# Optimization experiments

Hardware: AMD Instinct MI355X
Metric: run time of the kernel (lower is better)

## Reference

```python
import jax, jax.numpy as jnp
import numpy as np

B, C, H, W = 8, 512, 64, 64


def _conv1x1(x, w, b):
    # x: (B,C,H,W), w: (O,C,1,1) torch layout, b: (O,)
    y = jnp.einsum('bchw,oc->bohw', x, w[:, :, 0, 0])
    return y + b[None, :, None, None]


def setup_inputs() -> dict:
    key = jax.random.key(0)
    ks = jax.random.split(key, 9)
    s = 1.0 / np.sqrt(C)
    inp = {
        'x': jax.random.normal(ks[0], (B, C, H, W), dtype=jnp.float32),
        'w1': jax.random.uniform(ks[1], (C, C, 1, 1), jnp.float32, -s, s),
        'b1': jax.random.uniform(ks[2], (C,), jnp.float32, -s, s),
        'w2': jax.random.uniform(ks[3], (C, C, 1, 1), jnp.float32, -s, s),
        'b2': jax.random.uniform(ks[4], (C,), jnp.float32, -s, s),
        'w3': jax.random.uniform(ks[5], (C, C, 1, 1), jnp.float32, -s, s),
        'b3': jax.random.uniform(ks[6], (C,), jnp.float32, -s, s),
        'wg': jax.random.uniform(ks[7], (C, 1, 3, 3), jnp.float32, -1.0 / 3.0, 1.0 / 3.0),
        'bg': jax.random.uniform(ks[8], (C,), jnp.float32, -1.0 / 3.0, 1.0 / 3.0),
    }
    return inp


def reference(x, w1, b1, w2, b2, w3, b3, wg, bg):
    q = _conv1x1(x, w1, b1)  # (B,C,H,W)
    k = _conv1x1(x, w2, b2)
    v = _conv1x1(x, w3, b3)
    qf = q.reshape(B, C, H * W)
    kf = k.reshape(B, C, H * W)
    vf = v.reshape(B, C, H * W)
    # channel-wise attention: (B,C,C)
    scores = jnp.einsum('bcn,bdn->bcd', qf, kf)
    attn = jax.nn.softmax(scores, axis=-1)
    denoised = jnp.einsum('bcd,bdn->bcn', attn, vf).reshape(B, C, H, W)
    # depthwise 3x3 conv, padding=1
    local = jax.lax.conv_general_dilated(
        x, wg, window_strides=(1, 1), padding=((1, 1), (1, 1)),
        feature_group_count=C,
        dimension_numbers=('NCHW', 'OIHW', 'NCHW'))
    local = local + bg[None, :, None, None]
    return x + 0.1 * denoised + 0.1 * local
```

## Files before the change

### kernel.cpp

```cpp
#include <hip/hip_runtime.h>

typedef _Float16 f16;
typedef _Float16 half8 __attribute__((ext_vector_type(8)));
typedef _Float16 half4 __attribute__((ext_vector_type(4)));
typedef float    f32x4 __attribute__((ext_vector_type(4)));

#define DEV static __device__ __forceinline__

constexpr int NB = 8, CH = 512, HW = 4096, IH = 64, IW = 64;

typedef const __attribute__((address_space(1))) void gas_void;
typedef __attribute__((address_space(3))) void       las_void;

template <int ROWS>
DEV void stage_gll(f16* lds, const f16* src, long ld) {
  const int lane = threadIdx.x & 63, w = threadIdx.x >> 6;
  const int r8 = lane >> 3, c16 = lane & 7;
#pragma unroll
  for (int i = w; i < (ROWS / 8); i += 4) {
    const f16* g = src + (long)(i * 8 + r8) * ld + c16 * 8;
    __builtin_amdgcn_global_load_lds((gas_void*)g, (las_void*)(lds + i * 512 + lane * 8), 16, 0, 0);
  }
}

template <int BM, int BN, bool SPLIT, int KS, int EPI>
__global__ __launch_bounds__(256, 2) void gemm2(
    const f16* __restrict__ Ah, const f16* __restrict__ Al, long sAb, int lda,
    const f16* __restrict__ Bh, const f16* __restrict__ Bl, long sBb, int ldb,
    void* __restrict__ O1, void* __restrict__ O2, long sOb, int ldo, int K,
    const float* __restrict__ e0, const float* __restrict__ e1,
    const float* __restrict__ e2, const float* __restrict__ e3) {
  constexpr int FM = BM / 32, FN = BN / 32;
  __shared__ f16 sAh[BM * 64], sBh[BN * 64];
  __shared__ f16 sAl[SPLIT ? BM * 64 : 1], sBl[SPLIT ? BN * 64 : 1];

  const int bx = blockIdx.x, by = blockIdx.y;
  const int bz = blockIdx.z, b = bz / KS, ks = bz % KS;
  const int m0 = bx * BM, n0 = by * BN;
  const int lane = threadIdx.x & 63, wave = threadIdx.x >> 6;
  const int wr = (wave >> 1) * (BM / 2), wc = (wave & 1) * (BN / 2);
  const int fr = lane & 15, fq = lane >> 4;

  const f16* Ab  = Ah + b * sAb + (long)m0 * lda;
  const f16* Bb  = Bh + b * sBb + (long)n0 * ldb;
  const f16* Ab2 = SPLIT ? Al + b * sAb + (long)m0 * lda : nullptr;
  const f16* Bb2 = SPLIT ? Bl + b * sBb + (long)n0 * ldb : nullptr;

  f32x4 acc[FM][FN] = {};
  const int kbeg = ks * K, kend = kbeg + K;
  for (int k0 = kbeg; k0 < kend; k0 += 64) {
    stage_gll<BM>(sAh, Ab + k0, lda);
    stage_gll<BN>(sBh, Bb + k0, ldb);
    if constexpr (SPLIT) {
      stage_gll<BM>(sAl, Ab2 + k0, lda);
      stage_gll<BN>(sBl, Bb2 + k0, ldb);
    }
    __syncthreads();
#pragma unroll
    for (int kk = 0; kk < 2; ++kk) {
      half8 ah[FM], bh[FN];
#pragma unroll
      for (int mi = 0; mi < FM; ++mi)
        ah[mi] = *(const half8*)&sAh[(wr + mi * 16 + fr) * 64 + kk * 32 + fq * 8];
#pragma unroll
      for (int ni = 0; ni < FN; ++ni)
        bh[ni] = *(const half8*)&sBh[(wc + ni * 16 + fr) * 64 + kk * 32 + fq * 8];
      if constexpr (SPLIT) {
        half8 al[FM], bl[FN];
#pragma unroll
        for (int mi = 0; mi < FM; ++mi)
          al[mi] = *(const half8*)&sAl[(wr + mi * 16 + fr) * 64 + kk * 32 + fq * 8];
#pragma unroll
        for (int ni = 0; ni < FN; ++ni)
          bl[ni] = *(const half8*)&sBl[(wc + ni * 16 + fr) * 64 + kk * 32 + fq * 8];
#pragma unroll
        for (int mi = 0; mi < FM; ++mi)
#pragma unroll
          for (int ni = 0; ni < FN; ++ni) {
            acc[mi][ni] = __builtin_amdgcn_mfma_f32_16x16x32_f16(ah[mi], bh[ni], acc[mi][ni], 0, 0, 0);
            acc[mi][ni] = __builtin_amdgcn_mfma_f32_16x16x32_f16(ah[mi], bl[ni], acc[mi][ni], 0, 0, 0);
            acc[mi][ni] = __builtin_amdgcn_mfma_f32_16x16x32_f16(al[mi], bh[ni], acc[mi][ni], 0, 0, 0);
          }
      } else {
#pragma unroll
        for (int mi = 0; mi < FM; ++mi)
#pragma unroll
          for (int ni = 0; ni < FN; ++ni)
            acc[mi][ni] = __builtin_amdgcn_mfma_f32_16x16x32_f16(ah[mi], bh[ni], acc[mi][ni], 0, 0, 0);
      }
    }
    __syncthreads();
  }

#pragma unroll
  for (int mi = 0; mi < FM; ++mi)
#pragma unroll
    for (int ni = 0; ni < FN; ++ni)
#pragma unroll
      for (int j = 0; j < 4; ++j) {
        const int row = m0 + wr + mi * 16 + fq * 4 + j;
        const int col = n0 + wc + ni * 16 + fr;
        float g = acc[mi][ni][j];
        const long oi = b * sOb + (long)row * ldo + col;
        if constexpr (EPI == 0) {
          f16 h = (f16)g;
          ((f16*)O1)[oi] = h;
          ((f16*)O2)[oi] = (f16)(g - (float)h);
        } else if constexpr (EPI == 1) {
          g += e0[row] * e1[b * CH + col] + e2[b * CH + row] * e3[col];
          ((float*)O1)[oi] = g;
        } else if constexpr (EPI == 2) {
          ((f16*)O1)[oi] = (f16)g;
        } else {
          ((float*)O1)[(((long)ks * NB + b) * CH + row) * CH + col] = g;
        }
      }
}

template <int OP>
DEV float blockReduce(float v) {
#pragma unroll
  for (int o = 32; o; o >>= 1) {
    float w = __shfl_xor(v, o);
    v = OP ? fmaxf(v, w) : v + w;
  }
  __shared__ float t[4];
  __shared__ float res;
  __syncthreads();
  if ((threadIdx.x & 63) == 0) t[threadIdx.x >> 6] = v;
  __syncthreads();
  if (threadIdx.x == 0)
    res = OP ? fmaxf(fmaxf(t[0], t[1]), fmaxf(t[2], t[3])) : t[0] + t[1] + t[2] + t[3];
  __syncthreads();
  return res;
}

__global__ __launch_bounds__(256) void convert1(const float* __restrict__ x, f16* __restrict__ xh,
                                                f16* __restrict__ xm, float* __restrict__ sv) {
  const int c = blockIdx.x, b = blockIdx.y;
  const long base = ((long)(b * CH + c)) * HW;
  const float* p = x + base;
  f16* ph = xh + base;
  f16* pm = xm + base;
  float s = 0.f;
#pragma unroll
  for (int i0 = 0; i0 < 4; ++i0) {
    const int i = (threadIdx.x + i0 * 256) * 4;
    f32x4 v = *(const f32x4*)(p + i);
    half4 h, m;
#pragma unroll
    for (int j = 0; j < 4; ++j) {
      f16 hi = (f16)v[j];
      h[j] = hi;
      m[j] = (f16)(2.f * v[j] - (float)hi);
      s += v[j];
    }
    *(half4*)(ph + i) = h;
    *(half4*)(pm + i) = m;
  }
  s = blockReduce<0>(s);
  if (threadIdx.x == 0) sv[b * CH + c] = s;
}

__global__ __launch_bounds__(256) void convert2(const f16* __restrict__ xh, f16* __restrict__ xT) {
  const int p0 = blockIdx.x * 64, c0 = blockIdx.y * 64, b = blockIdx.z;
  __shared__ f16 tl[64][72];
  const int t = threadIdx.x;
  const int cr = t >> 2, pc = (t & 3) * 16;
  const f16* src = xh + ((long)(b * CH) + c0 + cr) * HW + p0 + pc;
  half8 a0 = *(const half8*)src, a1 = *(const half8*)(src + 8);
#pragma unroll
  for (int j = 0; j < 8; ++j) {
    tl[pc + j][cr] = a0[j];
    tl[pc + 8 + j][cr] = a1[j];
  }
  __syncthreads();
  f16* dst = xT + ((long)b * HW + p0 + cr) * CH + c0 + pc;
  *(half8*)dst       = *(half8*)&tl[cr][pc];
  *(half8*)(dst + 8) = *(half8*)&tl[cr][pc + 8];
}

template <int KS>
__global__ __launch_bounds__(256) void cvt_g(const float* __restrict__ E, f16* __restrict__ Gh,
                                             f16* __restrict__ Gl) {
  const int c0 = blockIdx.x * 64, r0 = blockIdx.y * 64, b = blockIdx.z;
  __shared__ float tl[64][65];
  const int t = threadIdx.x;
  const int rr0 = t >> 4, c4 = (t & 15) * 4;
  f32x4 acc[4] = {};
  for (int ks = 0; ks < KS; ++ks) {
    const float* Eb = E + ((long)ks * NB + b) * (long)CH * CH;
#pragma unroll
    for (int i = 0; i < 4; ++i)
      acc[i] += *(const f32x4*)(Eb + (long)(r0 + rr0 + i * 16) * CH + c0 + c4);
    __syncthreads();
#pragma unroll
    for (int i = 0; i < 4; ++i) {
      f32x4 w = *(const f32x4*)(Eb + (long)(c0 + rr0 + i * 16) * CH + r0 + c4);
#pragma unroll
      for (int j = 0; j < 4; ++j) tl[rr0 + i * 16][c4 + j] = w[j];
    }
    __syncthreads();
#pragma unroll
    for (int i = 0; i < 4; ++i)
#pragma unroll
      for (int j = 0; j < 4; ++j) acc[i][j] += tl[c4 + j][rr0 + i * 16];
  }
#pragma unroll
  for (int i = 0; i < 4; ++i) {
    half4 h, l;
#pragma unroll
    for (int j = 0; j < 4; ++j) {
      const float g = 0.5f * acc[i][j];
      f16 hi = (f16)g;
      h[j] = hi;
      l[j] = (f16)(g - (float)hi);
    }
    const long oi = ((long)b * CH + r0 + rr0 + i * 16) * CH + c0 + c4;
    *(half4*)(Gh + oi) = h;
    *(half4*)(Gl + oi) = l;
  }
}

__global__ __launch_bounds__(256) void prep_w(const float* __restrict__ w1, const float* __restrict__ w2,
                                              const float* __restrict__ w3, f16* w1h, f16* w1l, f16* w2h,
                                              f16* w2l, f16* w3t) {
  const int i = blockIdx.x * 256 + threadIdx.x;
  if (i >= CH * CH) return;
  float a = w1[i];
  f16 h = (f16)a;
  w1h[i] = h;
  w1l[i] = (f16)(a - (float)h);
  float bv = w2[i];
  h = (f16)bv;
  w2h[i] = h;
  w2l[i] = (f16)(bv - (float)h);
  const int r = i >> 9, c = i & 511;
  w3t[c * CH + r] = (f16)w3[i];
}

__global__ __launch_bounds__(256) void prep_tu(const float* __restrict__ w1, const float* __restrict__ w2,
                                               const float* __restrict__ b2, const float* __restrict__ s,
                                               float* __restrict__ t, float* __restrict__ u) {
  const int b = blockIdx.y, c = blockIdx.x;
  float a1 = 0.f, a2 = 0.f;
  for (int i = threadIdx.x; i < CH; i += 256) {
    float sv = s[b * CH + i];
    a1 += w1[(long)c * CH + i] * sv;
    a2 += w2[(long)c * CH + i] * sv;
  }
  a1 = blockReduce<0>(a1);
  a2 = blockReduce<0>(a2);
  if (threadIdx.x == 0) {
    t[b * CH + c] = a1;
    u[b * CH + c] = a2 + (float)HW * b2[c];
  }
}

__global__ __launch_bounds__(256) void softmax_k(const float* __restrict__ sc, const float* __restrict__ b3,
                                                 f16* __restrict__ attn, float* __restrict__ ab3) {
  const int b = blockIdx.y, c = blockIdx.x;
  const float* row = sc + ((long)(b * CH + c)) * CH;
  const float v0 = row[threadIdx.x], v1 = row[threadIdx.x + 256];
  const float m = blockReduce<1>(fmaxf(v0, v1));
  const float q0 = __expf(v0 - m), q1 = __expf(v1 - m);
  const float sum = blockReduce<0>(q0 + q1);
  const float sb = blockReduce<0>(q0 * b3[threadIdx.x] + q1 * b3[threadIdx.x + 256]);
  const float inv = 1.f / sum;
  attn[((long)(b * CH + c)) * CH + threadIdx.x] = (f16)(q0 * inv);
  attn[((long)(b * CH + c)) * CH + threadIdx.x + 256] = (f16)(q1 * inv);
  if (threadIdx.x == 0) ab3[b * CH + c] = sb * inv;
}

__global__ __launch_bounds__(256) void combine_k(const float* __restrict__ x, const f16* __restrict__ den,
                                                 const float* __restrict__ wg, const float* __restrict__ bg,
                                                 const float* __restrict__ ab3, float* __restrict__ out) {
  const int b = blockIdx.y, c = blockIdx.x;
  __shared__ float img[IH][IW + 4];
  const long base = ((long)(b * CH + c)) * HW;
  const float* p = x + base;
  const int t = threadIdx.x;
  const int h0 = t >> 2, w0 = (t & 3) * 16;
#pragma unroll
  for (int k = 0; k < 4; ++k)
    *(f32x4*)&img[h0][w0 + 4 * k] = *(const f32x4*)(p + h0 * 64 + w0 + 4 * k);
  __syncthreads();
  float w[3][3];
#pragma unroll
  for (int k = 0; k < 9; ++k) w[k / 3][k % 3] = wg[c * 9 + k];
  const float bb = bg[c] + ab3[b * CH + c];
  const f16* dp = den + base;
  float* op = out + base;
#pragma unroll
  for (int k = 0; k < 4; ++k) {
    const int ww = w0 + 4 * k;
    half4 d4 = *(const half4*)(dp + h0 * 64 + ww);
    f32x4 o;
#pragma unroll
    for (int j = 0; j < 4; ++j) {
      const int wj = ww + j;
      float acc = bb + (float)d4[j];
#pragma unroll
      for (int dy = -1; dy <= 1; ++dy) {
        const int hh = h0 + dy;
        if (hh < 0 || hh >= IH) continue;
#pragma unroll
        for (int dx = -1; dx <= 1; ++dx) {
          const int cc2 = wj + dx;
          if (cc2 < 0 || cc2 >= IW) continue;
          acc += w[dy + 1][dx + 1] * img[hh][cc2];
        }
      }
      o[j] = img[h0][wj] + 0.1f * acc;
    }
    *(f32x4*)(op + h0 * 64 + ww) = o;
  }
}

extern "C" void kernel_launch(void* const* d_in, const int* in_sizes, int n_in, void* d_out, int out_size,
                              void* d_ws, size_t ws_size, hipStream_t stream) {
  const float* x  = (const float*)d_in[0];
  const float* w1 = (const float*)d_in[1];
  const float* b1 = (const float*)d_in[2];
  const float* w2 = (const float*)d_in[3];
  const float* b2 = (const float*)d_in[4];
  const float* w3 = (const float*)d_in[5];
  const float* b3 = (const float*)d_in[6];
  const float* wg = (const float*)d_in[7];
  const float* bg = (const float*)d_in[8];
  float* out = (float*)d_out;

  char* ws = (char*)d_ws;
  size_t off = 0;
  auto alloc = [&](size_t bytes) -> void* {
    void* p = ws + off;
    off += (bytes + 255) & ~(size_t)255;
    return p;
  };
  const long CC = (long)CH * CH;
  const long CHW = (long)CH * HW;
  constexpr int GKS = 4;
  f16* xh    = (f16*)alloc(NB * CHW * 2);
  f16* xm    = (f16*)alloc(NB * CHW * 2);
  float* Epart = (float*)alloc((long)GKS * NB * CC * 4);
  f16* G16h = (f16*)alloc(NB * CC * 2);
  f16* G16l = (f16*)alloc(NB * CC * 2);
  f16* P16h = (f16*)alloc(NB * CC * 2);
  f16* P16l = (f16*)alloc(NB * CC * 2);
  f16* w1h = (f16*)alloc(CC * 2);
  f16* w1l = (f16*)alloc(CC * 2);
  f16* w2h = (f16*)alloc(CC * 2);
  f16* w2l = (f16*)alloc(CC * 2);
  f16* w3t = (f16*)alloc(CC * 2);
  float* sv = (float*)alloc(NB * CH * 4);
  float* tv = (float*)alloc(NB * CH * 4);
  float* uv = (float*)alloc(NB * CH * 4);
  float* ab3 = (float*)alloc(NB * CH * 4);
  f16* xT     = (f16*)Epart;
  float* scores = (float*)xh;
  f16* attn16 = (f16*)((char*)xh + (NB * CC * 4));
  f16* M16    = (f16*)((char*)xh + (NB * CC * 4) + (NB * CC * 2));
  f16* den16  = xm;

  const dim3 blk(256);

  prep_w<<<dim3((CH * CH + 255) / 256), blk, 0, stream>>>(w1, w2, w3, w1h, w1l, w2h, w2l, w3t);
  convert1<<<dim3(CH, NB), blk, 0, stream>>>(x, xh, xm, sv);
  prep_tu<<<dim3(CH, NB), blk, 0, stream>>>(w1, w2, b2, sv, tv, uv);

  gemm2<128, 128, false, GKS, 6><<<dim3(4, 4, NB * GKS), blk, 0, stream>>>(
      xh, nullptr, CHW, HW, xm, nullptr, CHW, HW, Epart, nullptr, CC, CH, HW / GKS,
      nullptr, nullptr, nullptr, nullptr);
  cvt_g<GKS><<<dim3(8, 8, NB), blk, 0, stream>>>(Epart, G16h, G16l);
  convert2<<<dim3(HW / 64, CH / 64, NB), blk, 0, stream>>>(xh, xT);
  gemm2<128, 64, true, 1, 0><<<dim3(4, 8, NB), blk, 0, stream>>>(
      w1h, w1l, 0, CH, G16h, G16l, CC, CH, P16h, P16l, CC, CH, CH,
      nullptr, nullptr, nullptr, nullptr);
  gemm2<128, 64, true, 1, 1><<<dim3(4, 8, NB), blk, 0, stream>>>(
      P16h, P16l, CC, CH, w2h, w2l, 0, CH, scores, nullptr, CC, CH, CH, b1, uv, tv, b2);
  softmax_k<<<dim3(CH, NB), blk, 0, stream>>>(scores, b3, attn16, ab3);
  gemm2<128, 64, false, 1, 2><<<dim3(4, 8, NB), blk, 0, stream>>>(
      attn16, nullptr, CC, CH, w3t, nullptr, 0, CH, M16, nullptr, CC, CH, CH,
      nullptr, nullptr, nullptr, nullptr);
  gemm2<128, 128, false, 1, 2><<<dim3(4, HW / 128, NB), blk, 0, stream>>>(
      M16, nullptr, CC, CH, xT, nullptr, CHW, CH, den16, nullptr, CHW, HW, CH,
      nullptr, nullptr, nullptr, nullptr);
  combine_k<<<dim3(CH, NB), blk, 0, stream>>>(x, den16, wg, bg, ab3, out);
}
```

Baseline: 337.0 us.

## Fuse final denoise GEMM with depthwise conv and residual epilogue

Replaces the last GEMM plus separate combine kernel with a single kernel that computes the M·xT tile and then, in its epilogue, applies the depthwise 3x3 conv from fp16 x rows staged in LDS, adds bias and residual, and writes the output directly. This removes the fp16 intermediate den16 write/read and one launch. The depthwise conv now uses fp16 x instead of fp32, and the epilogue's output writes are strided per lane (column-major in MFMA layout), which may reduce coalescing. Workspace aliasing is shuffled to keep xh alive.

```diff
diff --git a/kernel.cpp b/kernel.cpp
--- a/kernel.cpp
+++ b/kernel.cpp
@@ -117,6 +117,96 @@
       }
 }
 
+__global__ __launch_bounds__(256, 2) void gemm_dw(
+    const f16* __restrict__ M16, const f16* __restrict__ xT, const f16* __restrict__ xh,
+    const float* __restrict__ x, const float* __restrict__ wg, const float* __restrict__ bg,
+    const float* __restrict__ ab3, float* __restrict__ out) {
+  __shared__ __align__(16) char smem[128 * 4 * 68 * 2];
+  __shared__ float swg[128][10];
+  __shared__ float sbb[128];
+  f16* sA  = (f16*)smem;
+  f16* sB  = (f16*)(smem + 128 * 64 * 2);
+  f16* xdw = (f16*)smem;
+
+  const int b = blockIdx.z;
+  const int c0 = blockIdx.x * 128, p0 = blockIdx.y * 128;
+  const int h0 = p0 >> 6;
+  const int lane = threadIdx.x & 63, wave = threadIdx.x >> 6;
+  const int wr = (wave >> 1) * 64, wc = (wave & 1) * 64;
+  const int fr = lane & 15, fq = lane >> 4;
+  const long CC = (long)CH * CH, CHW = (long)CH * HW;
+
+  for (int q = threadIdx.x; q < 128 * 9; q += 256)
+    swg[q / 9][q % 9] = wg[(c0 + q / 9) * 9 + q % 9];
+  for (int c = threadIdx.x; c < 128; c += 256)
+    sbb[c] = bg[c0 + c] + ab3[b * CH + c0 + c];
+
+  const f16* Ab = M16 + b * CC + (long)c0 * CH;
+  const f16* Bb = xT + b * CHW + (long)p0 * CH;
+
+  f32x4 acc[4][4] = {};
+  for (int k0 = 0; k0 < CH; k0 += 64) {
+    stage_gll<128>(sA, Ab + k0, CH);
+    stage_gll<128>(sB, Bb + k0, CH);
+    __syncthreads();
+#pragma unroll
+    for (int kk = 0; kk < 2; ++kk) {
+      half8 ah[4], bh[4];
+#pragma unroll
+      for (int mi = 0; mi < 4; ++mi)
+        ah[mi] = *(const half8*)&sA[(wr + mi * 16 + fr) * 64 + kk * 32 + fq * 8];
+#pragma unroll
+      for (int ni = 0; ni < 4; ++ni)
+        bh[ni] = *(const half8*)&sB[(wc + ni * 16 + fr) * 64 + kk * 32 + fq * 8];
+#pragma unroll
+      for (int mi = 0; mi < 4; ++mi)
+#pragma unroll
+        for (int ni = 0; ni < 4; ++ni)
+          acc[mi][ni] = __builtin_amdgcn_mfma_f32_16x16x32_f16(ah[mi], bh[ni], acc[mi][ni], 0, 0, 0);
+    }
+    __syncthreads();
+  }
+
+  for (int q = threadIdx.x; q < 128 * 4 * 16; q += 256) {
+    const int c = q >> 6, dy = (q >> 4) & 3, w4 = (q & 15) * 4;
+    const int hg = h0 - 1 + dy;
+    half4 v = {};
+    if (hg >= 0 && hg < IH)
+      v = *(const half4*)(xh + ((long)b * CH + c0 + c) * HW + hg * 64 + w4);
+    *(half4*)&xdw[(c * 4 + dy) * 68 + w4] = v;
+  }
+  __syncthreads();
+
+#pragma unroll
+  for (int mi = 0; mi < 4; ++mi)
+#pragma unroll
+    for (int j = 0; j < 4; ++j) {
+      const int ci = wr + mi * 16 + fq * 4 + j;
+      float wgt[9];
+#pragma unroll
+      for (int k = 0; k < 9; ++k) wgt[k] = swg[ci][k];
+      const float bb = sbb[ci];
+      const long rowbase = ((long)b * CH + c0 + ci) * HW + p0;
+#pragma unroll
+      for (int ni = 0; ni < 4; ++ni) {
+        const int px = wc + ni * 16 + fr;
+        const int h = px >> 6, w = px & 63;
+        float dw = 0.f;
+#pragma unroll
+        for (int dy = 0; dy < 3; ++dy)
+#pragma unroll
+          for (int dx = 0; dx < 3; ++dx) {
+            const int wx = w + dx - 1;
+            const float tap =
+                (wx >= 0 && wx < IW) ? (float)xdw[(ci * 4 + h + dy) * 68 + wx] : 0.f;
+            dw += wgt[dy * 3 + dx] * tap;
+          }
+        const float xv = x[rowbase + px];
+        out[rowbase + px] = xv + 0.1f * (acc[mi][ni][j] + bb + dw);
+      }
+    }
+}
+
 template <int OP>
 DEV float blockReduce(float v) {
 #pragma unroll
@@ -270,51 +360,6 @@
   attn[((long)(b * CH + c)) * CH + threadIdx.x] = (f16)(q0 * inv);
   attn[((long)(b * CH + c)) * CH + threadIdx.x + 256] = (f16)(q1 * inv);
   if (threadIdx.x == 0) ab3[b * CH + c] = sb * inv;
-}
-
-__global__ __launch_bounds__(256) void combine_k(const float* __restrict__ x, const f16* __restrict__ den,
-                                                 const float* __restrict__ wg, const float* __restrict__ bg,
-                                                 const float* __restrict__ ab3, float* __restrict__ out) {
-  const int b = blockIdx.y, c = blockIdx.x;
-  __shared__ float img[IH][IW + 4];
-  const long base = ((long)(b * CH + c)) * HW;
-  const float* p = x + base;
-  const int t = threadIdx.x;
-  const int h0 = t >> 2, w0 = (t & 3) * 16;
-#pragma unroll
-  for (int k = 0; k < 4; ++k)
-    *(f32x4*)&img[h0][w0 + 4 * k] = *(const f32x4*)(p + h0 * 64 + w0 + 4 * k);
-  __syncthreads();
-  float w[3][3];
-#pragma unroll
-  for (int k = 0; k < 9; ++k) w[k / 3][k % 3] = wg[c * 9 + k];
-  const float bb = bg[c] + ab3[b * CH + c];
-  const f16* dp = den + base;
-  float* op = out + base;
-#pragma unroll
-  for (int k = 0; k < 4; ++k) {
-    const int ww = w0 + 4 * k;
-    half4 d4 = *(const half4*)(dp + h0 * 64 + ww);
-    f32x4 o;
-#pragma unroll
-    for (int j = 0; j < 4; ++j) {
-      const int wj = ww + j;
-      float acc = bb + (float)d4[j];
-#pragma unroll
-      for (int dy = -1; dy <= 1; ++dy) {
-        const int hh = h0 + dy;
-        if (hh < 0 || hh >= IH) continue;
-#pragma unroll
-        for (int dx = -1; dx <= 1; ++dx) {
-          const int cc2 = wj + dx;
-          if (cc2 < 0 || cc2 >= IW) continue;
-          acc += w[dy + 1][dx + 1] * img[hh][cc2];
-        }
-      }
-      o[j] = img[h0][wj] + 0.1f * acc;
-    }
-    *(f32x4*)(op + h0 * 64 + ww) = o;
-  }
 }
 
 extern "C" void kernel_launch(void* const* d_in, const int* in_sizes, int n_in, void* d_out, int out_size,
@@ -356,11 +401,10 @@
   float* tv = (float*)alloc(NB * CH * 4);
   float* uv = (float*)alloc(NB * CH * 4);
   float* ab3 = (float*)alloc(NB * CH * 4);
-  f16* xT     = (f16*)Epart;
-  float* scores = (float*)xh;
-  f16* attn16 = (f16*)((char*)xh + (NB * CC * 4));
-  f16* M16    = (f16*)((char*)xh + (NB * CC * 4) + (NB * CC * 2));
-  f16* den16  = xm;
+  f16* xT = (f16*)Epart;
+  float* scores = (float*)xm;
+  f16* attn16 = (f16*)((char*)xm + (NB * CC * 4));
+  f16* M16    = (f16*)((char*)xm + (NB * CC * 4) + (NB * CC * 2));
 
   const dim3 blk(256);
 
@@ -382,8 +426,6 @@
   gemm2<128, 64, false, 1, 2><<<dim3(4, 8, NB), blk, 0, stream>>>(
       attn16, nullptr, CC, CH, w3t, nullptr, 0, CH, M16, nullptr, CC, CH, CH,
       nullptr, nullptr, nullptr, nullptr);
-  gemm2<128, 128, false, 1, 2><<<dim3(4, HW / 128, NB), blk, 0, stream>>>(
-      M16, nullptr, CC, CH, xT, nullptr, CHW, CH, den16, nullptr, CHW, HW, CH,
-      nullptr, nullptr, nullptr, nullptr);
-  combine_k<<<dim3(CH, NB), blk, 0, stream>>>(x, den16, wg, bg, ab3, out);
-}
+  gemm_dw<<<dim3(CH / 128, HW / 128, NB), blk, 0, stream>>>(
+      M16, xT, xh, x, wg, bg, ab3, out);
+}
```

Result: faster. 329.9 us (-2.1%).
